# Optimization experiments

Hardware: AMD Instinct MI355X
Metric: run time of the kernel (lower is better)

## Reference

```python
import jax, jax.numpy as jnp
import numpy as np

N_NODES = 50000


def _gcn_norm(edge_index, num_nodes):
    # Add self-loops (PyG GCNConv default, fill_value=1.0) and compute
    # symmetric normalization: norm_e = d^-1/2[row_e] * d^-1/2[col_e].
    loops = jnp.arange(num_nodes, dtype=edge_index.dtype)
    row = jnp.concatenate([edge_index[0], loops])
    col = jnp.concatenate([edge_index[1], loops])
    w = jnp.ones(row.shape[0], dtype=jnp.float32)
    deg = jax.ops.segment_sum(w, col, num_segments=num_nodes)
    dinv = jnp.where(deg > 0, jax.lax.rsqrt(deg), 0.0)
    norm = dinv[row] * w * dinv[col]
    return row, col, norm


def _gcn_conv(x, W, b, row, col, norm, num_nodes):
    h = x @ W                               # [N, out] dense GEMM
    msg = h[row] * norm[:, None]            # gather + scale  [E2, out]
    out = jax.ops.segment_sum(msg, col, num_segments=num_nodes)
    return out + b


def setup_inputs() -> dict:
    key = jax.random.key(0)
    k1, k2, k3, k4 = jax.random.split(key, 4)
    F, H, C, E = 512, 256, 64, 800000
    x = jax.random.normal(k1, (N_NODES, F), dtype=jnp.float32)
    edge_index = jax.random.randint(k2, (2, E), 0, N_NODES, dtype=jnp.int64)
    W1 = jax.random.normal(k3, (F, H), dtype=jnp.float32) * (1.0 / np.sqrt(F))
    b1 = jnp.zeros((H,), dtype=jnp.float32)
    W2 = jax.random.normal(k4, (H, C), dtype=jnp.float32) * (1.0 / np.sqrt(H))
    b2 = jnp.zeros((C,), dtype=jnp.float32)
    return {"x": x, "edge_index": edge_index, "W1": W1, "b1": b1, "W2": W2, "b2": b2}


def reference(x, edge_index, W1, b1, W2, b2):
    n = x.shape[0]
    row, col, norm = _gcn_norm(edge_index, n)
    h = _gcn_conv(x, W1, b1, row, col, norm, n)
    h = jax.nn.relu(h)                      # dropout is identity in eval
    out = _gcn_conv(h, W2, b2, row, col, norm, n)
    return out                              # do_omit_softmax=False -> Identity head
```

## Files before the change

### kernel.cpp

```cpp
#include <hip/hip_runtime.h>


typedef __bf16 bf16x8 __attribute__((ext_vector_type(8)));
typedef __bf16 bf16x4 __attribute__((ext_vector_type(4)));
typedef float  f32x4  __attribute__((ext_vector_type(4)));

#define N_NODES  50000
#define N_PAD    50048
#define ZERO_ROW 50000
#define F_IN     512
#define F_HID    256
#define F_OUT    64
#define SCAN_B   196

__global__ __launch_bounds__(256) void convw_kernel(
    const float* __restrict__ W, __bf16* __restrict__ WT, int K, int N)
{
    int i = blockIdx.x * blockDim.x + threadIdx.x;
    if (i >= N * K) return;
    int n = i / K, k = i - n * K;
    WT[i] = (__bf16)W[(size_t)k * N + n];
}

__global__ __launch_bounds__(256) void initsrc_kernel(
    int* __restrict__ srcidx, int n4)
{
    int i = blockIdx.x * blockDim.x + threadIdx.x;
    if (i < n4) {
        int4 v = make_int4(ZERO_ROW, ZERO_ROW, ZERO_ROW, ZERO_ROW);
        *(int4*)(srcidx + i * 4) = v;
    }
}

__global__ __launch_bounds__(256) void count_kernel(
    const int* __restrict__ col, int E, int Nn, int* __restrict__ cnt)
{
    int e = blockIdx.x * blockDim.x + threadIdx.x;
    if (e < E) {
        int c = col[e];
        if ((unsigned)c < (unsigned)Nn) atomicAdd(&cnt[c], 1);
    }
}

__global__ __launch_bounds__(256) void scan_partial_kernel(
    const int* __restrict__ cnt, int* __restrict__ bsum, int N)
{
    __shared__ int s[256];
    const int t = threadIdx.x;
    const int i = blockIdx.x * 256 + t;
    int v = (i < N) ? ((cnt[i] + 1 + 3) & ~3) : 0;
    s[t] = v;
    __syncthreads();
    #pragma unroll
    for (int off = 128; off > 0; off >>= 1) {
        if (t < off) s[t] += s[t + off];
        __syncthreads();
    }
    if (t == 0) bsum[blockIdx.x] = s[0];
}

__global__ __launch_bounds__(256) void scan_bsum_kernel(
    const int* __restrict__ bsum, int* __restrict__ bofs,
    int* __restrict__ offs, int N, int PB)
{
    __shared__ int s[256];
    const int t = threadIdx.x;
    int v = (t < PB) ? bsum[t] : 0;
    s[t] = v;
    __syncthreads();
    #pragma unroll
    for (int off = 1; off < 256; off <<= 1) {
        int u = (t >= off) ? s[t - off] : 0;
        __syncthreads();
        s[t] += u;
        __syncthreads();
    }
    if (t < PB) bofs[t] = s[t] - v;
    if (t == 255) offs[N] = s[255];
}

__global__ __launch_bounds__(256) void scan_fill_kernel(
    const int* __restrict__ cnt, const int* __restrict__ bofs,
    int* __restrict__ offs, float* __restrict__ dinv, int N)
{
    __shared__ int s[256];
    const int t = threadIdx.x;
    const int i = blockIdx.x * 256 + t;
    int c   = (i < N) ? cnt[i] + 1 : 0;
    int cap = (c + 3) & ~3;
    s[t] = cap;
    __syncthreads();
    #pragma unroll
    for (int off = 1; off < 256; off <<= 1) {
        int u = (t >= off) ? s[t - off] : 0;
        __syncthreads();
        s[t] += u;
        __syncthreads();
    }
    if (i < N) {
        offs[i] = bofs[blockIdx.x] + s[t] - cap;
        dinv[i] = rsqrtf((float)c);
    }
}

__global__ __launch_bounds__(256) void fill_kernel(
    const int* __restrict__ row, const int* __restrict__ col,
    int E, int Nn, const int* __restrict__ offs,
    int* __restrict__ fill, int* __restrict__ srcidx)
{
    int e = blockIdx.x * blockDim.x + threadIdx.x;
    if (e < E) {
        int c = col[e];
        int r = row[e];
        if ((unsigned)c < (unsigned)Nn && (unsigned)r < (unsigned)Nn) {
            int p = offs[c] + atomicAdd(&fill[c], 1);
            srcidx[p] = r;
        }
    } else {
        int i = e - E;
        if (i < Nn) {
            int p = offs[i] + atomicAdd(&fill[i], 1);
            srcidx[p] = i;
        }
    }
}

__global__ __launch_bounds__(256) void gemm1_kernel(
    const float* __restrict__ A, const __bf16* __restrict__ BT,
    const float* __restrict__ dinv, __bf16* __restrict__ C)
{
    constexpr int BK = 32;
    constexpr int LDT = BK + 8;
    __shared__ __bf16 As[64 * LDT];
    __shared__ __bf16 Bs[256 * LDT];

    const int tid  = threadIdx.x;
    const int lane = tid & 63;
    const int wid  = tid >> 6;
    const int wm = wid >> 1, wn = wid & 1;
    const int bm = blockIdx.x * 64;
    const int lr = lane & 15, kg = lane >> 4;

    const int ar   = tid >> 2;
    const int achk = (tid & 3) * 8;
    const bool arow_ok = (bm + ar) < N_NODES;
    const float4* ap = (const float4*)(A + (size_t)(bm + ar) * F_IN + achk);
    const bf16x8* bp = (const bf16x8*)(BT + (size_t)tid * F_IN);

    f32x4 acc[2][8] = {};

    for (int k0 = 0; k0 < F_IN; k0 += BK) {
        float4 fa[2];
        if (arow_ok) {
            const float4* p = ap + (k0 >> 2);
            fa[0] = p[0]; fa[1] = p[1];
        } else {
            fa[0] = make_float4(0.f, 0.f, 0.f, 0.f);
            fa[1] = fa[0];
        }
        bf16x8 rb[4];
        {
            const bf16x8* q = bp + (k0 >> 3);
            rb[0] = q[0]; rb[1] = q[1]; rb[2] = q[2]; rb[3] = q[3];
        }
        __syncthreads();
        bf16x8 wa;
        wa[0]=(__bf16)fa[0].x; wa[1]=(__bf16)fa[0].y; wa[2]=(__bf16)fa[0].z; wa[3]=(__bf16)fa[0].w;
        wa[4]=(__bf16)fa[1].x; wa[5]=(__bf16)fa[1].y; wa[6]=(__bf16)fa[1].z; wa[7]=(__bf16)fa[1].w;
        *(bf16x8*)(As + ar * LDT + achk) = wa;
        #pragma unroll
        for (int j = 0; j < 4; ++j)
            *(bf16x8*)(Bs + tid * LDT + j * 8) = rb[j];
        __syncthreads();

        bf16x8 af[2], bfr[8];
        #pragma unroll
        for (int m = 0; m < 2; ++m)
            af[m] = *(const bf16x8*)(As + (wm * 32 + m * 16 + lr) * LDT + kg * 8);
        #pragma unroll
        for (int n = 0; n < 8; ++n)
            bfr[n] = *(const bf16x8*)(Bs + (wn * 128 + n * 16 + lr) * LDT + kg * 8);
        #pragma unroll
        for (int m = 0; m < 2; ++m)
            #pragma unroll
            for (int n = 0; n < 8; ++n)
                acc[m][n] = __builtin_amdgcn_mfma_f32_16x16x32_bf16(
                    af[m], bfr[n], acc[m][n], 0, 0, 0);
    }

    const int crow0 = bm + wm * 32 + kg * 4;
    const int ccol0 = wn * 128 + lr;
    #pragma unroll
    for (int m = 0; m < 2; ++m) {
        #pragma unroll
        for (int j = 0; j < 4; ++j) {
            int r = crow0 + m * 16 + j;
            float dv = (r < N_NODES) ? dinv[r] : 0.f;
            #pragma unroll
            for (int n = 0; n < 8; ++n)
                C[(size_t)r * F_HID + (ccol0 + n * 16)] = (__bf16)(dv * acc[m][n][j]);
        }
    }
}

template<int WGM, int WGN, int FM, int FN>
__global__ __launch_bounds__(256) void gemm_kernel(
    const __bf16* __restrict__ A, const __bf16* __restrict__ BT,
    const float* __restrict__ dinv, __bf16* __restrict__ C, int K, int N)
{
    constexpr int BM = WGM * FM * 16;
    constexpr int BN = WGN * FN * 16;
    constexpr int BK = 32;
    constexpr int LDT = BK + 8;
    __shared__ __bf16 As[BM * LDT];
    __shared__ __bf16 Bs[BN * LDT];

    const int tid  = threadIdx.x;
    const int lane = tid & 63;
    const int wid  = tid >> 6;
    const int wm = wid / WGN, wn = wid % WGN;
    const int bm = blockIdx.x * BM;
    const int bn = blockIdx.y * BN;
    const int lr = lane & 15, kg = lane >> 4;

    const int arow = tid >> 2;
    const int achk = (tid & 3) * 8;

    f32x4 acc[FM][FN] = {};

    for (int k0 = 0; k0 < K; k0 += BK) {
        bf16x8 ra[BM / 64], rb[BN / 64];
        #pragma unroll
        for (int p = 0; p < BM / 64; ++p)
            ra[p] = *(const bf16x8*)(A + (size_t)(bm + p * 64 + arow) * K + k0 + achk);
        #pragma unroll
        for (int p = 0; p < BN / 64; ++p)
            rb[p] = *(const bf16x8*)(BT + (size_t)(bn + p * 64 + arow) * K + k0 + achk);
        __syncthreads();
        #pragma unroll
        for (int p = 0; p < BM / 64; ++p)
            *(bf16x8*)(As + (p * 64 + arow) * LDT + achk) = ra[p];
        #pragma unroll
        for (int p = 0; p < BN / 64; ++p)
            *(bf16x8*)(Bs + (p * 64 + arow) * LDT + achk) = rb[p];
        __syncthreads();

        bf16x8 af[FM], bfv[FN];
        #pragma unroll
        for (int m = 0; m < FM; ++m)
            af[m] = *(const bf16x8*)(As + (wm * FM * 16 + m * 16 + lr) * LDT + kg * 8);
        #pragma unroll
        for (int n = 0; n < FN; ++n)
            bfv[n] = *(const bf16x8*)(Bs + (wn * FN * 16 + n * 16 + lr) * LDT + kg * 8);
        #pragma unroll
        for (int m = 0; m < FM; ++m)
            #pragma unroll
            for (int n = 0; n < FN; ++n)
                acc[m][n] = __builtin_amdgcn_mfma_f32_16x16x32_bf16(
                    af[m], bfv[n], acc[m][n], 0, 0, 0);
    }

    const int crow0 = bm + wm * FM * 16 + kg * 4;
    const int ccol0 = bn + wn * FN * 16 + lr;
    #pragma unroll
    for (int m = 0; m < FM; ++m) {
        #pragma unroll
        for (int j = 0; j < 4; ++j) {
            int r = crow0 + m * 16 + j;
            float dv = (r < N_NODES) ? dinv[r] : 0.f;
            #pragma unroll
            for (int n = 0; n < FN; ++n)
                C[(size_t)r * N + (ccol0 + n * 16)] = (__bf16)(dv * acc[m][n][j]);
        }
    }
}

template<int F, int FP, bool RELU, bool BF16OUT>
__global__ __launch_bounds__(256) void agg_kernel(
    const __bf16* __restrict__ H,
    const int* __restrict__ offs, const int* __restrict__ srcidx,
    const float* __restrict__ dinv, const float* __restrict__ bias,
    __bf16* __restrict__ outb, float* __restrict__ outf,
    int Nn, int Mpad)
{
    const int lane = threadIdx.x & 63;
    const int node = blockIdx.x * 4 + (threadIdx.x >> 6);
    if (node >= Mpad) return;
    if (node >= Nn) {
        if (BF16OUT) {
            #pragma unroll
            for (int j = 0; j < FP; ++j)
                outb[(size_t)node * F + lane * FP + j] = (__bf16)0.f;
        }
        return;
    }
    const int e0 = offs[node], e1 = offs[node + 1];
    const float dv = dinv[node];
    float acc[FP] = {};
    for (int e = e0; e < e1; e += 4) {
        int4 ss = *(const int4*)(srcidx + e);
        if constexpr (FP == 4) {
            bf16x4 v0 = *(const bf16x4*)(H + (size_t)ss.x * F + lane * 4);
            bf16x4 v1 = *(const bf16x4*)(H + (size_t)ss.y * F + lane * 4);
            bf16x4 v2 = *(const bf16x4*)(H + (size_t)ss.z * F + lane * 4);
            bf16x4 v3 = *(const bf16x4*)(H + (size_t)ss.w * F + lane * 4);
            #pragma unroll
            for (int j = 0; j < 4; ++j)
                acc[j] += (float)v0[j] + (float)v1[j] + (float)v2[j] + (float)v3[j];
        } else {
            __bf16 v0 = H[(size_t)ss.x * F + lane];
            __bf16 v1 = H[(size_t)ss.y * F + lane];
            __bf16 v2 = H[(size_t)ss.z * F + lane];
            __bf16 v3 = H[(size_t)ss.w * F + lane];
            acc[0] += (float)v0 + (float)v1 + (float)v2 + (float)v3;
        }
    }
    if constexpr (BF16OUT) {
        bf16x4 ov;
        #pragma unroll
        for (int j = 0; j < FP; ++j) {
            float r = dv * acc[j] + bias[lane * FP + j];
            if (RELU) r = fmaxf(r, 0.f);
            if constexpr (FP == 4) ov[j] = (__bf16)r;
            else outb[(size_t)node * F + lane] = (__bf16)r;
        }
        if constexpr (FP == 4)
            *(bf16x4*)(outb + (size_t)node * F + lane * 4) = ov;
    } else {
        #pragma unroll
        for (int j = 0; j < FP; ++j) {
            float r = dv * acc[j] + bias[lane * FP + j];
            if (RELU) r = fmaxf(r, 0.f);
            outf[(size_t)node * F + lane * FP + j] = r;
        }
    }
}

extern "C" void kernel_launch(void* const* d_in, const int* in_sizes, int n_in,
                              void* d_out, int out_size, void* d_ws, size_t ws_size,
                              hipStream_t stream)
{
    const float* x   = (const float*)d_in[0];
    const int*   ei  = (const int*)d_in[1];
    const float* W1  = (const float*)d_in[2];
    const float* b1  = (const float*)d_in[3];
    const float* W2  = (const float*)d_in[4];
    const float* b2  = (const float*)d_in[5];
    const int E  = in_sizes[1] / 2;
    const int Nn = N_NODES;
    const int E2 = E + Nn;
    const int E2P = E + 4 * Nn;
    const int* rowp = ei;
    const int* colp = ei + E;

    char* w = (char*)d_ws;
    auto alloc = [&](size_t bytes) {
        char* p = w; w += (bytes + 255) & ~(size_t)255; return p;
    };
    __bf16* h1   = (__bf16*)alloc((size_t)N_PAD * F_HID * 2);
    __bf16* h2   = (__bf16*)alloc((size_t)N_PAD * F_HID * 2);
    __bf16* w1t  = (__bf16*)alloc((size_t)F_HID * F_IN  * 2);
    __bf16* w2t  = (__bf16*)alloc((size_t)F_OUT * F_HID * 2);
    int*    cnt  = (int*)  alloc((size_t)Nn * 4);
    int*    fil  = (int*)  alloc((size_t)Nn * 4);
    int*    offs = (int*)  alloc((size_t)(Nn + 1) * 4);
    float*  dinv = (float*)alloc((size_t)Nn * 4);
    int*    bsum = (int*)  alloc((size_t)SCAN_B * 4);
    int*    bofs = (int*)  alloc((size_t)SCAN_B * 4);
    int*    srcx = (int*)  alloc((size_t)E2P * 4);
    __bf16* t2 = h1;

    hipMemsetAsync(cnt, 0, (size_t)Nn * 4, stream);
    hipMemsetAsync(fil, 0, (size_t)Nn * 4, stream);
    initsrc_kernel<<<(E2P / 4 + 255) / 256, 256, 0, stream>>>(srcx, E2P / 4);

    convw_kernel<<<(F_IN * F_HID + 255) / 256, 256, 0, stream>>>(W1, w1t, F_IN, F_HID);
    convw_kernel<<<(F_HID * F_OUT + 255) / 256, 256, 0, stream>>>(W2, w2t, F_HID, F_OUT);

    count_kernel<<<(E + 255) / 256, 256, 0, stream>>>(colp, E, Nn, cnt);
    scan_partial_kernel<<<SCAN_B, 256, 0, stream>>>(cnt, bsum, Nn);
    scan_bsum_kernel<<<1, 256, 0, stream>>>(bsum, bofs, offs, Nn, SCAN_B);
    scan_fill_kernel<<<SCAN_B, 256, 0, stream>>>(cnt, bofs, offs, dinv, Nn);
    fill_kernel<<<(E2 + 255) / 256, 256, 0, stream>>>(rowp, colp, E, Nn, offs, fil, srcx);

    gemm1_kernel<<<N_PAD / 64, 256, 0, stream>>>(x, w1t, dinv, h1);
    agg_kernel<F_HID, 4, true, true><<<N_PAD / 4, 256, 0, stream>>>(
        h1, offs, srcx, dinv, b1, h2, nullptr, Nn, N_PAD);

    gemm_kernel<4, 1, 1, 4><<<dim3(N_PAD / 64, 1), 256, 0, stream>>>(
        h2, w2t, dinv, t2, F_HID, F_OUT);
    agg_kernel<F_OUT, 1, false, false><<<(Nn + 3) / 4, 256, 0, stream>>>(
        t2, offs, srcx, dinv, b2, nullptr, (float*)d_out, Nn, Nn);
}
```

Baseline: 390.1 us.

## Register-prefetch GEMM1 without LDS, vectorize CSR build, unroll aggregation by 8

GEMM1 stops staging tiles through shared memory. Each wave now loads its A and B fragments straight from global memory into registers, prefetching several k-chunks ahead, and launch bounds request 2 blocks per CU. The count and fill kernels each handle 4 edges per thread using int4 loads, and CSR bucket padding rises from 4 to 8 so the aggregation loop can gather 8 neighbours per iteration for more memory-level parallelism. The risks are more padded zero-row gathers, redundant global loads of B across waves without LDS reuse, higher register pressure in GEMM1, and the int4 load in count_kernel assuming E is divisible by 4 and aligned.

```diff
diff --git a/kernel.cpp b/kernel.cpp
--- a/kernel.cpp
+++ b/kernel.cpp
@@ -35,11 +35,13 @@
 __global__ __launch_bounds__(256) void count_kernel(
     const int* __restrict__ col, int E, int Nn, int* __restrict__ cnt)
 {
-    int e = blockIdx.x * blockDim.x + threadIdx.x;
-    if (e < E) {
-        int c = col[e];
-        if ((unsigned)c < (unsigned)Nn) atomicAdd(&cnt[c], 1);
-    }
+    int e0 = (blockIdx.x * blockDim.x + threadIdx.x) * 4;
+    if (e0 >= E) return;
+    int4 cc = *(const int4*)(col + e0);
+    if ((unsigned)cc.x < (unsigned)Nn) atomicAdd(&cnt[cc.x], 1);
+    if ((unsigned)cc.y < (unsigned)Nn) atomicAdd(&cnt[cc.y], 1);
+    if ((unsigned)cc.z < (unsigned)Nn) atomicAdd(&cnt[cc.z], 1);
+    if ((unsigned)cc.w < (unsigned)Nn) atomicAdd(&cnt[cc.w], 1);
 }
 
 __global__ __launch_bounds__(256) void scan_partial_kernel(
@@ -48,7 +50,7 @@
     __shared__ int s[256];
     const int t = threadIdx.x;
     const int i = blockIdx.x * 256 + t;
-    int v = (i < N) ? ((cnt[i] + 1 + 3) & ~3) : 0;
+    int v = (i < N) ? ((cnt[i] + 1 + 7) & ~7) : 0;
     s[t] = v;
     __syncthreads();
     #pragma unroll
@@ -87,7 +89,7 @@
     const int t = threadIdx.x;
     const int i = blockIdx.x * 256 + t;
     int c   = (i < N) ? cnt[i] + 1 : 0;
-    int cap = (c + 3) & ~3;
+    int cap = (c + 7) & ~7;
     s[t] = cap;
     __syncthreads();
     #pragma unroll
@@ -108,32 +110,30 @@
     int E, int Nn, const int* __restrict__ offs,
     int* __restrict__ fill, int* __restrict__ srcidx)
 {
-    int e = blockIdx.x * blockDim.x + threadIdx.x;
-    if (e < E) {
-        int c = col[e];
-        int r = row[e];
+    int e0 = (blockIdx.x * blockDim.x + threadIdx.x) * 4;
+    int total = E + Nn;
+    if (e0 >= total) return;
+    int rr[4], cc[4];
+    #pragma unroll
+    for (int j = 0; j < 4; ++j) {
+        int e = e0 + j;
+        if (e < E)      { cc[j] = col[e]; rr[j] = row[e]; }
+        else            { int i = e - E; cc[j] = (i < Nn) ? i : -1; rr[j] = cc[j]; }
+    }
+    #pragma unroll
+    for (int j = 0; j < 4; ++j) {
+        int c = cc[j], r = rr[j];
         if ((unsigned)c < (unsigned)Nn && (unsigned)r < (unsigned)Nn) {
             int p = offs[c] + atomicAdd(&fill[c], 1);
             srcidx[p] = r;
         }
-    } else {
-        int i = e - E;
-        if (i < Nn) {
-            int p = offs[i] + atomicAdd(&fill[i], 1);
-            srcidx[p] = i;
-        }
-    }
-}
-
-__global__ __launch_bounds__(256) void gemm1_kernel(
+    }
+}
+
+__global__ __launch_bounds__(256, 2) void gemm1_kernel(
     const float* __restrict__ A, const __bf16* __restrict__ BT,
     const float* __restrict__ dinv, __bf16* __restrict__ C)
 {
-    constexpr int BK = 32;
-    constexpr int LDT = BK + 8;
-    __shared__ __bf16 As[64 * LDT];
-    __shared__ __bf16 Bs[256 * LDT];
-
     const int tid  = threadIdx.x;
     const int lane = tid & 63;
     const int wid  = tid >> 6;
@@ -141,52 +141,53 @@
     const int bm = blockIdx.x * 64;
     const int lr = lane & 15, kg = lane >> 4;
 
-    const int ar   = tid >> 2;
-    const int achk = (tid & 3) * 8;
-    const bool arow_ok = (bm + ar) < N_NODES;
-    const float4* ap = (const float4*)(A + (size_t)(bm + ar) * F_IN + achk);
-    const bf16x8* bp = (const bf16x8*)(BT + (size_t)tid * F_IN);
-
-    f32x4 acc[2][8] = {};
-
-    for (int k0 = 0; k0 < F_IN; k0 += BK) {
-        float4 fa[2];
-        if (arow_ok) {
-            const float4* p = ap + (k0 >> 2);
-            fa[0] = p[0]; fa[1] = p[1];
-        } else {
-            fa[0] = make_float4(0.f, 0.f, 0.f, 0.f);
-            fa[1] = fa[0];
-        }
-        bf16x8 rb[4];
-        {
-            const bf16x8* q = bp + (k0 >> 3);
-            rb[0] = q[0]; rb[1] = q[1]; rb[2] = q[2]; rb[3] = q[3];
-        }
-        __syncthreads();
-        bf16x8 wa;
-        wa[0]=(__bf16)fa[0].x; wa[1]=(__bf16)fa[0].y; wa[2]=(__bf16)fa[0].z; wa[3]=(__bf16)fa[0].w;
-        wa[4]=(__bf16)fa[1].x; wa[5]=(__bf16)fa[1].y; wa[6]=(__bf16)fa[1].z; wa[7]=(__bf16)fa[1].w;
-        *(bf16x8*)(As + ar * LDT + achk) = wa;
-        #pragma unroll
-        for (int j = 0; j < 4; ++j)
-            *(bf16x8*)(Bs + tid * LDT + j * 8) = rb[j];
-        __syncthreads();
-
-        bf16x8 af[2], bfr[8];
-        #pragma unroll
-        for (int m = 0; m < 2; ++m)
-            af[m] = *(const bf16x8*)(As + (wm * 32 + m * 16 + lr) * LDT + kg * 8);
-        #pragma unroll
-        for (int n = 0; n < 8; ++n)
-            bfr[n] = *(const bf16x8*)(Bs + (wn * 128 + n * 16 + lr) * LDT + kg * 8);
+    const int row0 = bm + wm * 32 + lr;
+    const int row1 = row0 + 16;
+    const int r0c = (row0 < N_NODES) ? row0 : 0;
+    const int r1c = (row1 < N_NODES) ? row1 : 0;
+    const float*  pa0 = A  + (size_t)r0c * F_IN + kg * 8;
+    const float*  pa1 = A  + (size_t)r1c * F_IN + kg * 8;
+    const __bf16* pb  = BT + (size_t)(wn * 128 + lr) * F_IN + kg * 8;
+
+    float4 fa[4][2][2];
+    bf16x8 fb[2][8];
+    f32x4  acc[2][8] = {};
+
+#define LA(i) {                                                    \
+        fa[(i) & 3][0][0] = *(const float4*)(pa0 + (i) * 32);      \
+        fa[(i) & 3][0][1] = *(const float4*)(pa0 + (i) * 32 + 4);  \
+        fa[(i) & 3][1][0] = *(const float4*)(pa1 + (i) * 32);      \
+        fa[(i) & 3][1][1] = *(const float4*)(pa1 + (i) * 32 + 4); }
+#define LB(i) {                                                    \
+        _Pragma("unroll")                                          \
+        for (int n = 0; n < 8; ++n)                                \
+            fb[(i) & 1][n] = *(const bf16x8*)(pb + (size_t)n * 16 * F_IN + (i) * 32); }
+
+    LA(0) LA(1) LA(2)
+    LB(0)
+
+    #pragma unroll
+    for (int kc = 0; kc < 16; ++kc) {
+        if (kc + 3 < 16) LA(kc + 3)
+        if (kc + 1 < 16) LB(kc + 1)
+        bf16x8 wa[2];
+        #pragma unroll
+        for (int m = 0; m < 2; ++m) {
+            float4 x0 = fa[kc & 3][m][0], x1 = fa[kc & 3][m][1];
+            wa[m][0]=(__bf16)x0.x; wa[m][1]=(__bf16)x0.y;
+            wa[m][2]=(__bf16)x0.z; wa[m][3]=(__bf16)x0.w;
+            wa[m][4]=(__bf16)x1.x; wa[m][5]=(__bf16)x1.y;
+            wa[m][6]=(__bf16)x1.z; wa[m][7]=(__bf16)x1.w;
+        }
         #pragma unroll
         for (int m = 0; m < 2; ++m)
             #pragma unroll
             for (int n = 0; n < 8; ++n)
                 acc[m][n] = __builtin_amdgcn_mfma_f32_16x16x32_bf16(
-                    af[m], bfr[n], acc[m][n], 0, 0, 0);
-    }
+                    wa[m], fb[kc & 1][n], acc[m][n], 0, 0, 0);
+    }
+#undef LA
+#undef LB
 
     const int crow0 = bm + wm * 32 + kg * 4;
     const int ccol0 = wn * 128 + lr;
@@ -297,22 +298,33 @@
     const int e0 = offs[node], e1 = offs[node + 1];
     const float dv = dinv[node];
     float acc[FP] = {};
-    for (int e = e0; e < e1; e += 4) {
-        int4 ss = *(const int4*)(srcidx + e);
+    for (int e = e0; e < e1; e += 8) {
+        int4 sa = *(const int4*)(srcidx + e);
+        int4 sb = *(const int4*)(srcidx + e + 4);
         if constexpr (FP == 4) {
-            bf16x4 v0 = *(const bf16x4*)(H + (size_t)ss.x * F + lane * 4);
-            bf16x4 v1 = *(const bf16x4*)(H + (size_t)ss.y * F + lane * 4);
-            bf16x4 v2 = *(const bf16x4*)(H + (size_t)ss.z * F + lane * 4);
-            bf16x4 v3 = *(const bf16x4*)(H + (size_t)ss.w * F + lane * 4);
+            bf16x4 v0 = *(const bf16x4*)(H + (size_t)sa.x * F + lane * 4);
+            bf16x4 v1 = *(const bf16x4*)(H + (size_t)sa.y * F + lane * 4);
+            bf16x4 v2 = *(const bf16x4*)(H + (size_t)sa.z * F + lane * 4);
+            bf16x4 v3 = *(const bf16x4*)(H + (size_t)sa.w * F + lane * 4);
+            bf16x4 v4 = *(const bf16x4*)(H + (size_t)sb.x * F + lane * 4);
+            bf16x4 v5 = *(const bf16x4*)(H + (size_t)sb.y * F + lane * 4);
+            bf16x4 v6 = *(const bf16x4*)(H + (size_t)sb.z * F + lane * 4);
+            bf16x4 v7 = *(const bf16x4*)(H + (size_t)sb.w * F + lane * 4);
             #pragma unroll
             for (int j = 0; j < 4; ++j)
-                acc[j] += (float)v0[j] + (float)v1[j] + (float)v2[j] + (float)v3[j];
+                acc[j] += ((float)v0[j] + (float)v1[j] + (float)v2[j] + (float)v3[j])
+                        + ((float)v4[j] + (float)v5[j] + (float)v6[j] + (float)v7[j]);
         } else {
-            __bf16 v0 = H[(size_t)ss.x * F + lane];
-            __bf16 v1 = H[(size_t)ss.y * F + lane];
-            __bf16 v2 = H[(size_t)ss.z * F + lane];
-            __bf16 v3 = H[(size_t)ss.w * F + lane];
-            acc[0] += (float)v0 + (float)v1 + (float)v2 + (float)v3;
+            __bf16 v0 = H[(size_t)sa.x * F + lane];
+            __bf16 v1 = H[(size_t)sa.y * F + lane];
+            __bf16 v2 = H[(size_t)sa.z * F + lane];
+            __bf16 v3 = H[(size_t)sa.w * F + lane];
+            __bf16 v4 = H[(size_t)sb.x * F + lane];
+            __bf16 v5 = H[(size_t)sb.y * F + lane];
+            __bf16 v6 = H[(size_t)sb.z * F + lane];
+            __bf16 v7 = H[(size_t)sb.w * F + lane];
+            acc[0] += ((float)v0 + (float)v1 + (float)v2 + (float)v3)
+                    + ((float)v4 + (float)v5 + (float)v6 + (float)v7);
         }
     }
     if constexpr (BF16OUT) {
@@ -348,8 +360,7 @@
     const float* b2  = (const float*)d_in[5];
     const int E  = in_sizes[1] / 2;
     const int Nn = N_NODES;
-    const int E2 = E + Nn;
-    const int E2P = E + 4 * Nn;
+    const int E2P = E + 8 * Nn;
     const int* rowp = ei;
     const int* colp = ei + E;
 
@@ -377,11 +388,12 @@
     convw_kernel<<<(F_IN * F_HID + 255) / 256, 256, 0, stream>>>(W1, w1t, F_IN, F_HID);
     convw_kernel<<<(F_HID * F_OUT + 255) / 256, 256, 0, stream>>>(W2, w2t, F_HID, F_OUT);
 
-    count_kernel<<<(E + 255) / 256, 256, 0, stream>>>(colp, E, Nn, cnt);
+    count_kernel<<<(E / 4 + 255) / 256, 256, 0, stream>>>(colp, E, Nn, cnt);
     scan_partial_kernel<<<SCAN_B, 256, 0, stream>>>(cnt, bsum, Nn);
     scan_bsum_kernel<<<1, 256, 0, stream>>>(bsum, bofs, offs, Nn, SCAN_B);
     scan_fill_kernel<<<SCAN_B, 256, 0, stream>>>(cnt, bofs, offs, dinv, Nn);
-    fill_kernel<<<(E2 + 255) / 256, 256, 0, stream>>>(rowp, colp, E, Nn, offs, fil, srcx);
+    fill_kernel<<<((E + Nn) / 4 + 255) / 256, 256, 0, stream>>>(
+        rowp, colp, E, Nn, offs, fil, srcx);
 
     gemm1_kernel<<<N_PAD / 64, 256, 0, stream>>>(x, w1t, dinv, h1);
     agg_kernel<F_HID, 4, true, true><<<N_PAD / 4, 256, 0, stream>>>(
```

Result: slower. 431.5 us (+10.6%).
